# Optimization experiments

Hardware: AMD Instinct MI355X
Metric: run time of the kernel (lower is better)

The kernel has to match this reference:

```python
import jax, jax.numpy as jnp
import numpy as np

NUM_CLASSES = 50000
FEAT_DIM = 256
BATCH = 131072
LAMBDA_CENT = 0.5
EPS = 1e-12  # matches F.normalize default eps


def setup_inputs() -> dict:
    key = jax.random.key(0)
    k1, k2, k3 = jax.random.split(key, 3)
    features = jax.random.normal(k1, (BATCH, FEAT_DIM), dtype=jnp.float32)
    labels = jax.random.randint(k2, (BATCH,), 0, NUM_CLASSES)
    centers = jax.random.normal(k3, (NUM_CLASSES, FEAT_DIM), dtype=jnp.float32)
    return {"features": features, "labels": labels, "centers": centers}


def reference(features, labels, centers):
    # L2 normalize rows (F.normalize, p=2, dim=1)
    norms = jnp.linalg.norm(features, axis=1, keepdims=True)
    f = features / jnp.maximum(norms, EPS)
    # gather centers per sample: [B, D]
    cb = centers[labels]
    loss_cent = jnp.sum((f - cb) ** 2) / features.shape[0]
    # training-mode center update, vectorized:
    # torch loop: delta[labels[i]] += (cb[i] - f[i]) / (1 + count(labels == labels[i]))
    cnt = jax.ops.segment_sum(jnp.ones(labels.shape, f.dtype), labels,
                              num_segments=NUM_CLASSES)  # [C]
    w = 1.0 / (1.0 + cnt[labels])  # [B]
    delta = jax.ops.segment_sum((cb - f) * w[:, None], labels,
                                num_segments=NUM_CLASSES)  # [C, D]
    new_centers = centers - LAMBDA_CENT * delta
    return loss_cent, new_centers
```

## Files before the change

kernel.cpp:

```cpp
#include <hip/hip_runtime.h>
#include <hip/hip_bf16.h>
#include <math.h>

#define BATCH   131072
#define FEAT    256
#define NCLASS  50000
#define EPS     1e-12f
#define LAMBDA  0.5f
#define CAP     32

constexpr int WPB     = 4;
constexpr int NBLK_NS = BATCH  / WPB;
constexpr int NBLK_SS = NCLASS / WPB;
constexpr int NSCAN   = (NCLASS + 255) / 256;


__device__ __forceinline__ float wave_reduce_sum(float v) {
    #pragma unroll
    for (int m = 32; m; m >>= 1) v += __shfl_xor(v, m, 64);
    return v;
}

__device__ __forceinline__ unsigned int pack_bf16(float a, float b) {
    union { __hip_bfloat162 h; unsigned int u; } cvt;
    cvt.h = __float22bfloat162_rn(make_float2(a, b));
    return cvt.u;
}

__device__ __forceinline__ float2 unpack_bf16(unsigned int u) {
    union { unsigned int u; __hip_bfloat162 h; } cvt;
    cvt.u = u;
    return __bfloat1622float2(cvt.h);
}

__global__ __launch_bounds__(256) void histo(const int* __restrict__ labels,
                                             int* __restrict__ cnt) {
    const int i = blockIdx.x * 256 + threadIdx.x;
    atomicAdd(&cnt[labels[i]], 1);
}

__global__ __launch_bounds__(256) void scan_bsum(const int* __restrict__ cnt,
                                                 int* __restrict__ bsum) {
    __shared__ int s[256];
    const int i = blockIdx.x * 256 + threadIdx.x;
    s[threadIdx.x] = (i < NCLASS) ? cnt[i] : 0;
    __syncthreads();
    for (int off = 128; off; off >>= 1) {
        if (threadIdx.x < off) s[threadIdx.x] += s[threadIdx.x + off];
        __syncthreads();
    }
    if (threadIdx.x == 0) bsum[blockIdx.x] = s[0];
}

__global__ __launch_bounds__(256) void scan_boff(const int* __restrict__ bsum,
                                                 int* __restrict__ boff) {
    __shared__ int s[256];
    const int t = threadIdx.x;
    const int v = (t < NSCAN) ? bsum[t] : 0;
    s[t] = v;
    __syncthreads();
    for (int off = 1; off < 256; off <<= 1) {
        int u = (t >= off) ? s[t - off] : 0;
        __syncthreads();
        s[t] += u;
        __syncthreads();
    }
    if (t < NSCAN) boff[t] = s[t] - v;
}

__global__ __launch_bounds__(256) void scan_final(const int* __restrict__ cnt,
                                                  const int* __restrict__ boff,
                                                  int* __restrict__ cursor) {
    __shared__ int s[256];
    const int t = threadIdx.x;
    const int i = blockIdx.x * 256 + t;
    const int v = (i < NCLASS) ? cnt[i] : 0;
    s[t] = v;
    __syncthreads();
    for (int off = 1; off < 256; off <<= 1) {
        int u = (t >= off) ? s[t - off] : 0;
        __syncthreads();
        s[t] += u;
        __syncthreads();
    }
    if (i < NCLASS) cursor[i] = s[t] - v + boff[blockIdx.x];
}

__global__ __launch_bounds__(256) void normalize_scatter(
        const float* __restrict__ feat,
        const int*   __restrict__ labels,
        int*         __restrict__ cursor,
        uint2*       __restrict__ sortedH,
        float*       __restrict__ pA) {
    const int wave = threadIdx.x >> 6;
    const int lane = threadIdx.x & 63;
    const int row  = blockIdx.x * WPB + wave;

    const float4 v = ((const float4*)(feat + (size_t)row * FEAT))[lane];
    const float ss = wave_reduce_sum(v.x*v.x + v.y*v.y + v.z*v.z + v.w*v.w);
    const float rinv = 1.0f / fmaxf(sqrtf(ss), EPS);

    int slot = 0;
    if (lane == 0) slot = atomicAdd(&cursor[labels[row]], 1);
    slot = __shfl(slot, 0, 64);

    uint2 h;
    h.x = pack_bf16(v.x * rinv, v.y * rinv);
    h.y = pack_bf16(v.z * rinv, v.w * rinv);
    sortedH[(size_t)slot * 64 + lane] = h;

    __shared__ float red[WPB];
    if (lane == 0) red[wave] = ss * rinv * rinv;
    __syncthreads();
    if (threadIdx.x == 0)
        pA[blockIdx.x] = red[0] + red[1] + red[2] + red[3];
}

__global__ __launch_bounds__(256) void segsum_update(
        const uint2* __restrict__ sortedH,
        const float* __restrict__ centers,
        const int*   __restrict__ cnt,
        const int*   __restrict__ cursor_end,
        float*       __restrict__ outc,
        float*       __restrict__ pB) {
    const int wave = threadIdx.x >> 6;
    const int lane = threadIdx.x & 63;
    const int c    = blockIdx.x * WPB + wave;

    const int n     = cnt[c];
    const int start = cursor_end[c] - n;
    const uint2* base = sortedH + (size_t)start * 64;

    float4 acc = {0.f, 0.f, 0.f, 0.f};
    for (int s = 0; s < n; s += 4) {
        const int m = n - s;
        uint2 a0 = base[(size_t)(s + 0) * 64 + lane];
        uint2 a1 = {0u,0u}, a2 = {0u,0u}, a3 = {0u,0u};
        if (m > 1) a1 = base[(size_t)(s + 1) * 64 + lane];
        if (m > 2) a2 = base[(size_t)(s + 2) * 64 + lane];
        if (m > 3) a3 = base[(size_t)(s + 3) * 64 + lane];

        const float2 x0 = unpack_bf16(a0.x), y0 = unpack_bf16(a0.y);
        const float2 x1 = unpack_bf16(a1.x), y1 = unpack_bf16(a1.y);
        const float2 x2 = unpack_bf16(a2.x), y2 = unpack_bf16(a2.y);
        const float2 x3 = unpack_bf16(a3.x), y3 = unpack_bf16(a3.y);
        acc.x += (x0.x + x1.x) + (x2.x + x3.x);
        acc.y += (x0.y + x1.y) + (x2.y + x3.y);
        acc.z += (y0.x + y1.x) + (y2.x + y3.x);
        acc.w += (y0.y + y1.y) + (y2.y + y3.y);
    }

    const float4 cv = ((const float4*)(centers + (size_t)c * FEAT))[lane];
    const float fn = (float)n;
    const float w  = 1.0f / (1.0f + fn);

    float4 nc;
    nc.x = cv.x - LAMBDA * (fn * cv.x - acc.x) * w;
    nc.y = cv.y - LAMBDA * (fn * cv.y - acc.y) * w;
    nc.z = cv.z - LAMBDA * (fn * cv.z - acc.z) * w;
    nc.w = cv.w - LAMBDA * (fn * cv.w - acc.w) * w;
    ((float4*)(outc + (size_t)c * FEAT))[lane] = nc;

    float lp = fn * (cv.x*cv.x + cv.y*cv.y + cv.z*cv.z + cv.w*cv.w)
             - 2.0f * (acc.x*cv.x + acc.y*cv.y + acc.z*cv.z + acc.w*cv.w);
    lp = wave_reduce_sum(lp);

    __shared__ float red[WPB];
    if (lane == 0) red[wave] = lp;
    __syncthreads();
    if (threadIdx.x == 0)
        pB[blockIdx.x] = red[0] + red[1] + red[2] + red[3];
}

__global__ __launch_bounds__(1024) void finish(const float* __restrict__ pA,
                                               const float* __restrict__ pB,
                                               float* __restrict__ out0) {
    float s = 0.0f;
    for (int i = threadIdx.x; i < NBLK_NS; i += 1024) s += pA[i];
    for (int i = threadIdx.x; i < NBLK_SS; i += 1024) s += pB[i];
    s = wave_reduce_sum(s);
    __shared__ float red[16];
    const int wave = threadIdx.x >> 6;
    const int lane = threadIdx.x & 63;
    if (lane == 0) red[wave] = s;
    __syncthreads();
    if (threadIdx.x == 0) {
        float t = 0.0f;
        #pragma unroll
        for (int i = 0; i < 16; ++i) t += red[i];
        out0[0] = t * (1.0f / (float)BATCH);
    }
}


__global__ __launch_bounds__(256) void scatter_bucket(const int* __restrict__ labels,
                                                      int* __restrict__ cnt,
                                                      int* __restrict__ bucket) {
    const int i = blockIdx.x * 256 + threadIdx.x;
    const int c = labels[i];
    const int slot = atomicAdd(&cnt[c], 1);
    if (slot < CAP) bucket[c * CAP + slot] = i;
}

__global__ __launch_bounds__(256) void gather_bucket(
        const float* __restrict__ feat, const float* __restrict__ centers,
        const int* __restrict__ cnt, const int* __restrict__ bucket,
        float* __restrict__ outc, float* __restrict__ pB) {
    const int wave = threadIdx.x >> 6;
    const int lane = threadIdx.x & 63;
    const int c    = blockIdx.x * WPB + wave;
    const int n = min(cnt[c], CAP);
    const int myidx = (lane < n) ? bucket[c * CAP + lane] : 0;
    float4 acc = {0.f,0.f,0.f,0.f};
    float fsum2 = 0.f;
    for (int s = 0; s < n; ++s) {
        const int r = __shfl(myidx, s, 64);
        const float4 v = ((const float4*)(feat + (size_t)r * FEAT))[lane];
        float ss = wave_reduce_sum(v.x*v.x + v.y*v.y + v.z*v.z + v.w*v.w);
        const float rinv = 1.0f / fmaxf(sqrtf(ss), EPS);
        acc.x += v.x*rinv; acc.y += v.y*rinv; acc.z += v.z*rinv; acc.w += v.w*rinv;
        fsum2 += ss * rinv * rinv;
    }
    const float4 cv = ((const float4*)(centers + (size_t)c * FEAT))[lane];
    const float fn = (float)n;
    const float w  = 1.0f / (1.0f + fn);
    float4 nc;
    nc.x = cv.x - LAMBDA * (fn*cv.x - acc.x) * w;
    nc.y = cv.y - LAMBDA * (fn*cv.y - acc.y) * w;
    nc.z = cv.z - LAMBDA * (fn*cv.z - acc.z) * w;
    nc.w = cv.w - LAMBDA * (fn*cv.w - acc.w) * w;
    ((float4*)(outc + (size_t)c * FEAT))[lane] = nc;
    float lp = fn * (cv.x*cv.x + cv.y*cv.y + cv.z*cv.z + cv.w*cv.w)
             - 2.0f * (acc.x*cv.x + acc.y*cv.y + acc.z*cv.z + acc.w*cv.w);
    lp = wave_reduce_sum(lp);
    __shared__ float red[WPB];
    if (lane == 0) red[wave] = lp + fsum2;
    __syncthreads();
    if (threadIdx.x == 0)
        pB[blockIdx.x] = red[0] + red[1] + red[2] + red[3];
}

__global__ __launch_bounds__(1024) void finishB(const float* __restrict__ pB,
                                                float* __restrict__ out0) {
    float s = 0.0f;
    for (int i = threadIdx.x; i < NBLK_SS; i += 1024) s += pB[i];
    s = wave_reduce_sum(s);
    __shared__ float red[16];
    const int wave = threadIdx.x >> 6;
    const int lane = threadIdx.x & 63;
    if (lane == 0) red[wave] = s;
    __syncthreads();
    if (threadIdx.x == 0) {
        float t = 0.0f;
        #pragma unroll
        for (int i = 0; i < 16; ++i) t += red[i];
        out0[0] = t * (1.0f / (float)BATCH);
    }
}

extern "C" void kernel_launch(void* const* d_in, const int* in_sizes, int n_in,
                              void* d_out, int out_size, void* d_ws, size_t ws_size,
                              hipStream_t stream) {
    const float* feat    = (const float*)d_in[0];
    const int*   labels  = (const int*)  d_in[1];
    const float* centers = (const float*)d_in[2];
    float* out = (float*)d_out;

    const size_t hdr = (size_t)NCLASS * 2 + 512 + NBLK_NS + NBLK_SS;
    const size_t need_fast = hdr * 4 + (size_t)BATCH * FEAT * 2;

    if (ws_size >= need_fast) {
        int*   cnt     = (int*)d_ws;
        int*   cursor  = cnt + NCLASS;
        int*   bsum    = cursor + NCLASS;
        int*   boff    = bsum + 256;
        float* pA      = (float*)(boff + 256);
        float* pB      = pA + NBLK_NS;
        uint2* sortedH = (uint2*)(pB + NBLK_SS);

        hipMemsetAsync(cnt, 0, NCLASS * sizeof(int), stream);
        histo     <<<BATCH / 256, 256, 0, stream>>>(labels, cnt);
        scan_bsum <<<NSCAN, 256, 0, stream>>>(cnt, bsum);
        scan_boff <<<1, 256, 0, stream>>>(bsum, boff);
        scan_final<<<NSCAN, 256, 0, stream>>>(cnt, boff, cursor);
        normalize_scatter<<<NBLK_NS, 256, 0, stream>>>(feat, labels, cursor,
                                                       sortedH, pA);
        segsum_update<<<NBLK_SS, 256, 0, stream>>>(sortedH, centers, cnt, cursor,
                                                   out + 1, pB);
        finish<<<1, 1024, 0, stream>>>(pA, pB, out);
    } else {
        int*   cnt    = (int*)d_ws;
        int*   bucket = cnt + NCLASS;
        float* pB     = (float*)(bucket + (size_t)NCLASS * CAP);
        hipMemsetAsync(cnt, 0, NCLASS * sizeof(int), stream);
        scatter_bucket<<<BATCH / 256, 256, 0, stream>>>(labels, cnt, bucket);
        gather_bucket <<<NBLK_SS, 256, 0, stream>>>(feat, centers, cnt, bucket,
                                                    out + 1, pB);
        finishB<<<1, 1024, 0, stream>>>(pB, out);
    }
}
```

Baseline: 294.7 us.

## Sort row indices instead of normalized bf16 features and gather rows in segsum

Replaces the normalize-and-scatter pass, which wrote a bf16 copy of every normalized feature row into label-sorted order, with a light kernel that only scatters row indices. The per-class kernel now gathers fp32 feature rows by index, normalizes them in place with a wave reduction, and accumulates both the segment sum and the squared-norm loss term. This removes a full write and re-read of the intermediate feature buffer and the bf16 rounding, at the cost of random row gathers of fp32 data and extra shuffle reductions per row inside the segmented loop.

```diff
diff --git a/kernel.cpp b/kernel.cpp
--- a/kernel.cpp
+++ b/kernel.cpp
@@ -10,7 +10,6 @@
 #define CAP     32
 
 constexpr int WPB     = 4;
-constexpr int NBLK_NS = BATCH  / WPB;
 constexpr int NBLK_SS = NCLASS / WPB;
 constexpr int NSCAN   = (NCLASS + 255) / 256;
 
@@ -19,18 +18,6 @@
     #pragma unroll
     for (int m = 32; m; m >>= 1) v += __shfl_xor(v, m, 64);
     return v;
-}
-
-__device__ __forceinline__ unsigned int pack_bf16(float a, float b) {
-    union { __hip_bfloat162 h; unsigned int u; } cvt;
-    cvt.h = __float22bfloat162_rn(make_float2(a, b));
-    return cvt.u;
-}
-
-__device__ __forceinline__ float2 unpack_bf16(unsigned int u) {
-    union { unsigned int u; __hip_bfloat162 h; } cvt;
-    cvt.u = u;
-    return __bfloat1622float2(cvt.h);
 }
 
 __global__ __launch_bounds__(256) void histo(const int* __restrict__ labels,
@@ -86,41 +73,20 @@
     if (i < NCLASS) cursor[i] = s[t] - v + boff[blockIdx.x];
 }
 
-__global__ __launch_bounds__(256) void normalize_scatter(
+__global__ __launch_bounds__(256) void scatter_idx(const int* __restrict__ labels,
+                                                   int* __restrict__ cursor,
+                                                   int* __restrict__ sIdx) {
+    const int i = blockIdx.x * 256 + threadIdx.x;
+    const int slot = atomicAdd(&cursor[labels[i]], 1);
+    sIdx[slot] = i;
+}
+
+__global__ __launch_bounds__(256) void segsum_gather(
         const float* __restrict__ feat,
-        const int*   __restrict__ labels,
-        int*         __restrict__ cursor,
-        uint2*       __restrict__ sortedH,
-        float*       __restrict__ pA) {
-    const int wave = threadIdx.x >> 6;
-    const int lane = threadIdx.x & 63;
-    const int row  = blockIdx.x * WPB + wave;
-
-    const float4 v = ((const float4*)(feat + (size_t)row * FEAT))[lane];
-    const float ss = wave_reduce_sum(v.x*v.x + v.y*v.y + v.z*v.z + v.w*v.w);
-    const float rinv = 1.0f / fmaxf(sqrtf(ss), EPS);
-
-    int slot = 0;
-    if (lane == 0) slot = atomicAdd(&cursor[labels[row]], 1);
-    slot = __shfl(slot, 0, 64);
-
-    uint2 h;
-    h.x = pack_bf16(v.x * rinv, v.y * rinv);
-    h.y = pack_bf16(v.z * rinv, v.w * rinv);
-    sortedH[(size_t)slot * 64 + lane] = h;
-
-    __shared__ float red[WPB];
-    if (lane == 0) red[wave] = ss * rinv * rinv;
-    __syncthreads();
-    if (threadIdx.x == 0)
-        pA[blockIdx.x] = red[0] + red[1] + red[2] + red[3];
-}
-
-__global__ __launch_bounds__(256) void segsum_update(
-        const uint2* __restrict__ sortedH,
         const float* __restrict__ centers,
         const int*   __restrict__ cnt,
         const int*   __restrict__ cursor_end,
+        const int*   __restrict__ sIdx,
         float*       __restrict__ outc,
         float*       __restrict__ pB) {
     const int wave = threadIdx.x >> 6;
@@ -129,25 +95,53 @@
 
     const int n     = cnt[c];
     const int start = cursor_end[c] - n;
-    const uint2* base = sortedH + (size_t)start * 64;
-
-    float4 acc = {0.f, 0.f, 0.f, 0.f};
-    for (int s = 0; s < n; s += 4) {
-        const int m = n - s;
-        uint2 a0 = base[(size_t)(s + 0) * 64 + lane];
-        uint2 a1 = {0u,0u}, a2 = {0u,0u}, a3 = {0u,0u};
-        if (m > 1) a1 = base[(size_t)(s + 1) * 64 + lane];
-        if (m > 2) a2 = base[(size_t)(s + 2) * 64 + lane];
-        if (m > 3) a3 = base[(size_t)(s + 3) * 64 + lane];
-
-        const float2 x0 = unpack_bf16(a0.x), y0 = unpack_bf16(a0.y);
-        const float2 x1 = unpack_bf16(a1.x), y1 = unpack_bf16(a1.y);
-        const float2 x2 = unpack_bf16(a2.x), y2 = unpack_bf16(a2.y);
-        const float2 x3 = unpack_bf16(a3.x), y3 = unpack_bf16(a3.y);
-        acc.x += (x0.x + x1.x) + (x2.x + x3.x);
-        acc.y += (x0.y + x1.y) + (x2.y + x3.y);
-        acc.z += (y0.x + y1.x) + (y2.x + y3.x);
-        acc.w += (y0.y + y1.y) + (y2.y + y3.y);
+
+    float4 acc   = {0.f, 0.f, 0.f, 0.f};
+    float  fsum2 = 0.f;
+
+    for (int base = 0; base < n; base += 64) {
+        const int cn = min(64, n - base);
+        int myidx = 0;
+        if (lane < cn) myidx = sIdx[start + base + lane];
+
+        for (int s = 0; s < cn; s += 4) {
+            const int m  = cn - s;
+            const int r0 = __shfl(myidx, s + 0, 64);
+            const int r1 = __shfl(myidx, s + 1, 64);
+            const int r2 = __shfl(myidx, s + 2, 64);
+            const int r3 = __shfl(myidx, s + 3, 64);
+
+            const float4 v0 = ((const float4*)(feat + (size_t)r0 * FEAT))[lane];
+            float4 v1 = {0.f,0.f,0.f,0.f}, v2 = {0.f,0.f,0.f,0.f}, v3 = {0.f,0.f,0.f,0.f};
+            if (m > 1) v1 = ((const float4*)(feat + (size_t)r1 * FEAT))[lane];
+            if (m > 2) v2 = ((const float4*)(feat + (size_t)r2 * FEAT))[lane];
+            if (m > 3) v3 = ((const float4*)(feat + (size_t)r3 * FEAT))[lane];
+
+            float a0 = v0.x*v0.x + v0.y*v0.y + v0.z*v0.z + v0.w*v0.w;
+            float a1 = v1.x*v1.x + v1.y*v1.y + v1.z*v1.z + v1.w*v1.w;
+            float a2 = v2.x*v2.x + v2.y*v2.y + v2.z*v2.z + v2.w*v2.w;
+            float a3 = v3.x*v3.x + v3.y*v3.y + v3.z*v3.z + v3.w*v3.w;
+
+            #pragma unroll
+            for (int sh = 32; sh; sh >>= 1) {
+                a0 += __shfl_xor(a0, sh, 64);
+                a1 += __shfl_xor(a1, sh, 64);
+                a2 += __shfl_xor(a2, sh, 64);
+                a3 += __shfl_xor(a3, sh, 64);
+            }
+
+            const float i0 = 1.0f / fmaxf(sqrtf(a0), EPS);
+            const float i1 = 1.0f / fmaxf(sqrtf(a1), EPS);
+            const float i2 = 1.0f / fmaxf(sqrtf(a2), EPS);
+            const float i3 = 1.0f / fmaxf(sqrtf(a3), EPS);
+
+            acc.x += v0.x*i0 + v1.x*i1 + v2.x*i2 + v3.x*i3;
+            acc.y += v0.y*i0 + v1.y*i1 + v2.y*i2 + v3.y*i3;
+            acc.z += v0.z*i0 + v1.z*i1 + v2.z*i2 + v3.z*i3;
+            acc.w += v0.w*i0 + v1.w*i1 + v2.w*i2 + v3.w*i3;
+
+            fsum2 += (a0*i0)*i0 + (a1*i1)*i1 + (a2*i2)*i2 + (a3*i3)*i3;
+        }
     }
 
     const float4 cv = ((const float4*)(centers + (size_t)c * FEAT))[lane];
@@ -166,17 +160,15 @@
     lp = wave_reduce_sum(lp);
 
     __shared__ float red[WPB];
-    if (lane == 0) red[wave] = lp;
+    if (lane == 0) red[wave] = lp + fsum2;
     __syncthreads();
     if (threadIdx.x == 0)
         pB[blockIdx.x] = red[0] + red[1] + red[2] + red[3];
 }
 
-__global__ __launch_bounds__(1024) void finish(const float* __restrict__ pA,
-                                               const float* __restrict__ pB,
+__global__ __launch_bounds__(1024) void finish(const float* __restrict__ pB,
                                                float* __restrict__ out0) {
     float s = 0.0f;
-    for (int i = threadIdx.x; i < NBLK_NS; i += 1024) s += pA[i];
     for (int i = threadIdx.x; i < NBLK_SS; i += 1024) s += pB[i];
     s = wave_reduce_sum(s);
     __shared__ float red[16];
@@ -266,28 +258,25 @@
     const float* centers = (const float*)d_in[2];
     float* out = (float*)d_out;
 
-    const size_t hdr = (size_t)NCLASS * 2 + 512 + NBLK_NS + NBLK_SS;
-    const size_t need_fast = hdr * 4 + (size_t)BATCH * FEAT * 2;
+    const size_t need_fast = ((size_t)NCLASS * 2 + 512 + NBLK_SS + BATCH) * 4;
 
     if (ws_size >= need_fast) {
-        int*   cnt     = (int*)d_ws;
-        int*   cursor  = cnt + NCLASS;
-        int*   bsum    = cursor + NCLASS;
-        int*   boff    = bsum + 256;
-        float* pA      = (float*)(boff + 256);
-        float* pB      = pA + NBLK_NS;
-        uint2* sortedH = (uint2*)(pB + NBLK_SS);
+        int*   cnt    = (int*)d_ws;
+        int*   cursor = cnt + NCLASS;
+        int*   bsum   = cursor + NCLASS;
+        int*   boff   = bsum + 256;
+        float* pB     = (float*)(boff + 256);
+        int*   sIdx   = (int*)(pB + NBLK_SS);
 
         hipMemsetAsync(cnt, 0, NCLASS * sizeof(int), stream);
-        histo     <<<BATCH / 256, 256, 0, stream>>>(labels, cnt);
-        scan_bsum <<<NSCAN, 256, 0, stream>>>(cnt, bsum);
-        scan_boff <<<1, 256, 0, stream>>>(bsum, boff);
-        scan_final<<<NSCAN, 256, 0, stream>>>(cnt, boff, cursor);
-        normalize_scatter<<<NBLK_NS, 256, 0, stream>>>(feat, labels, cursor,
-                                                       sortedH, pA);
-        segsum_update<<<NBLK_SS, 256, 0, stream>>>(sortedH, centers, cnt, cursor,
-                                                   out + 1, pB);
-        finish<<<1, 1024, 0, stream>>>(pA, pB, out);
+        histo      <<<BATCH / 256, 256, 0, stream>>>(labels, cnt);
+        scan_bsum  <<<NSCAN, 256, 0, stream>>>(cnt, bsum);
+        scan_boff  <<<1, 256, 0, stream>>>(bsum, boff);
+        scan_final <<<NSCAN, 256, 0, stream>>>(cnt, boff, cursor);
+        scatter_idx<<<BATCH / 256, 256, 0, stream>>>(labels, cursor, sIdx);
+        segsum_gather<<<NBLK_SS, 256, 0, stream>>>(feat, centers, cnt, cursor,
+                                                   sIdx, out + 1, pB);
+        finish<<<1, 1024, 0, stream>>>(pB, out);
     } else {
         int*   cnt    = (int*)d_ws;
         int*   bucket = cnt + NCLASS;
```

Result: faster. 277.7 us (-5.8%).

## Scatter row indices and norms instead of bf16 rows; gather fp32 features in segsum

Applied to the files above, without the earlier changes.

The normalize kernel no longer writes a bf16 copy of every normalized row into a label-sorted buffer. It only records the row index and inverse norm per sorted slot. The segment-sum kernel then gathers the original fp32 feature rows by index, broadcasting indices through shuffles, and scales them by the stored inverse norm. This removes the 64MB bf16 write and re-read, but it adds a second 128MB random-gather read of the features. In exchange it improves precision by dropping the bf16 rounding.

```diff
diff --git a/kernel.cpp b/kernel.cpp
--- a/kernel.cpp
+++ b/kernel.cpp
@@ -19,18 +19,6 @@
     #pragma unroll
     for (int m = 32; m; m >>= 1) v += __shfl_xor(v, m, 64);
     return v;
-}
-
-__device__ __forceinline__ unsigned int pack_bf16(float a, float b) {
-    union { __hip_bfloat162 h; unsigned int u; } cvt;
-    cvt.h = __float22bfloat162_rn(make_float2(a, b));
-    return cvt.u;
-}
-
-__device__ __forceinline__ float2 unpack_bf16(unsigned int u) {
-    union { unsigned int u; __hip_bfloat162 h; } cvt;
-    cvt.u = u;
-    return __bfloat1622float2(cvt.h);
 }
 
 __global__ __launch_bounds__(256) void histo(const int* __restrict__ labels,
@@ -86,11 +74,12 @@
     if (i < NCLASS) cursor[i] = s[t] - v + boff[blockIdx.x];
 }
 
-__global__ __launch_bounds__(256) void normalize_scatter(
+__global__ __launch_bounds__(256) void norm_scatter(
         const float* __restrict__ feat,
         const int*   __restrict__ labels,
         int*         __restrict__ cursor,
-        uint2*       __restrict__ sortedH,
+        int*         __restrict__ sIdx,
+        float*       __restrict__ rinvS,
         float*       __restrict__ pA) {
     const int wave = threadIdx.x >> 6;
     const int lane = threadIdx.x & 63;
@@ -100,14 +89,11 @@
     const float ss = wave_reduce_sum(v.x*v.x + v.y*v.y + v.z*v.z + v.w*v.w);
     const float rinv = 1.0f / fmaxf(sqrtf(ss), EPS);
 
-    int slot = 0;
-    if (lane == 0) slot = atomicAdd(&cursor[labels[row]], 1);
-    slot = __shfl(slot, 0, 64);
-
-    uint2 h;
-    h.x = pack_bf16(v.x * rinv, v.y * rinv);
-    h.y = pack_bf16(v.z * rinv, v.w * rinv);
-    sortedH[(size_t)slot * 64 + lane] = h;
+    if (lane == 0) {
+        const int slot = atomicAdd(&cursor[labels[row]], 1);
+        sIdx[slot]  = row;
+        rinvS[slot] = rinv;
+    }
 
     __shared__ float red[WPB];
     if (lane == 0) red[wave] = ss * rinv * rinv;
@@ -116,11 +102,13 @@
         pA[blockIdx.x] = red[0] + red[1] + red[2] + red[3];
 }
 
-__global__ __launch_bounds__(256) void segsum_update(
-        const uint2* __restrict__ sortedH,
+__global__ __launch_bounds__(256) void segsum_gather2(
+        const float* __restrict__ feat,
         const float* __restrict__ centers,
         const int*   __restrict__ cnt,
         const int*   __restrict__ cursor_end,
+        const int*   __restrict__ sIdx,
+        const float* __restrict__ rinvS,
         float*       __restrict__ outc,
         float*       __restrict__ pB) {
     const int wave = threadIdx.x >> 6;
@@ -129,25 +117,30 @@
 
     const int n     = cnt[c];
     const int start = cursor_end[c] - n;
-    const uint2* base = sortedH + (size_t)start * 64;
 
     float4 acc = {0.f, 0.f, 0.f, 0.f};
-    for (int s = 0; s < n; s += 4) {
-        const int m = n - s;
-        uint2 a0 = base[(size_t)(s + 0) * 64 + lane];
-        uint2 a1 = {0u,0u}, a2 = {0u,0u}, a3 = {0u,0u};
-        if (m > 1) a1 = base[(size_t)(s + 1) * 64 + lane];
-        if (m > 2) a2 = base[(size_t)(s + 2) * 64 + lane];
-        if (m > 3) a3 = base[(size_t)(s + 3) * 64 + lane];
-
-        const float2 x0 = unpack_bf16(a0.x), y0 = unpack_bf16(a0.y);
-        const float2 x1 = unpack_bf16(a1.x), y1 = unpack_bf16(a1.y);
-        const float2 x2 = unpack_bf16(a2.x), y2 = unpack_bf16(a2.y);
-        const float2 x3 = unpack_bf16(a3.x), y3 = unpack_bf16(a3.y);
-        acc.x += (x0.x + x1.x) + (x2.x + x3.x);
-        acc.y += (x0.y + x1.y) + (x2.y + x3.y);
-        acc.z += (y0.x + y1.x) + (y2.x + y3.x);
-        acc.w += (y0.y + y1.y) + (y2.y + y3.y);
+
+    for (int base = 0; base < n; base += 64) {
+        const int cn = min(64, n - base);
+        int   myidx = 0;
+        float myrv  = 0.f;
+        if (lane < cn) {
+            myidx = sIdx [start + base + lane];
+            myrv  = rinvS[start + base + lane];
+        }
+
+        for (int s = 0; s < cn; s += 8) {
+            #pragma unroll
+            for (int k = 0; k < 8; ++k) {
+                const int   r  = __shfl(myidx, s + k, 64);
+                const float rv = __shfl(myrv,  s + k, 64);
+                const float4 v = ((const float4*)(feat + (size_t)r * FEAT))[lane];
+                acc.x += v.x * rv;
+                acc.y += v.y * rv;
+                acc.z += v.z * rv;
+                acc.w += v.w * rv;
+            }
+        }
     }
 
     const float4 cv = ((const float4*)(centers + (size_t)c * FEAT))[lane];
@@ -266,27 +259,28 @@
     const float* centers = (const float*)d_in[2];
     float* out = (float*)d_out;
 
-    const size_t hdr = (size_t)NCLASS * 2 + 512 + NBLK_NS + NBLK_SS;
-    const size_t need_fast = hdr * 4 + (size_t)BATCH * FEAT * 2;
+    const size_t need_fast =
+        ((size_t)NCLASS * 2 + 512 + NBLK_NS + NBLK_SS + (size_t)BATCH * 2) * 4;
 
     if (ws_size >= need_fast) {
-        int*   cnt     = (int*)d_ws;
-        int*   cursor  = cnt + NCLASS;
-        int*   bsum    = cursor + NCLASS;
-        int*   boff    = bsum + 256;
-        float* pA      = (float*)(boff + 256);
-        float* pB      = pA + NBLK_NS;
-        uint2* sortedH = (uint2*)(pB + NBLK_SS);
+        int*   cnt    = (int*)d_ws;
+        int*   cursor = cnt + NCLASS;
+        int*   bsum   = cursor + NCLASS;
+        int*   boff   = bsum + 256;
+        float* pA     = (float*)(boff + 256);
+        float* pB     = pA + NBLK_NS;
+        int*   sIdx   = (int*)(pB + NBLK_SS);
+        float* rinvS  = (float*)(sIdx + BATCH);
 
         hipMemsetAsync(cnt, 0, NCLASS * sizeof(int), stream);
-        histo     <<<BATCH / 256, 256, 0, stream>>>(labels, cnt);
-        scan_bsum <<<NSCAN, 256, 0, stream>>>(cnt, bsum);
-        scan_boff <<<1, 256, 0, stream>>>(bsum, boff);
-        scan_final<<<NSCAN, 256, 0, stream>>>(cnt, boff, cursor);
-        normalize_scatter<<<NBLK_NS, 256, 0, stream>>>(feat, labels, cursor,
-                                                       sortedH, pA);
-        segsum_update<<<NBLK_SS, 256, 0, stream>>>(sortedH, centers, cnt, cursor,
-                                                   out + 1, pB);
+        histo      <<<BATCH / 256, 256, 0, stream>>>(labels, cnt);
+        scan_bsum  <<<NSCAN, 256, 0, stream>>>(cnt, bsum);
+        scan_boff  <<<1, 256, 0, stream>>>(bsum, boff);
+        scan_final <<<NSCAN, 256, 0, stream>>>(cnt, boff, cursor);
+        norm_scatter<<<NBLK_NS, 256, 0, stream>>>(feat, labels, cursor,
+                                                  sIdx, rinvS, pA);
+        segsum_gather2<<<NBLK_SS, 256, 0, stream>>>(feat, centers, cnt, cursor,
+                                                    sIdx, rinvS, out + 1, pB);
         finish<<<1, 1024, 0, stream>>>(pA, pB, out);
     } else {
         int*   cnt    = (int*)d_ws;
```

Result: no change. 294.8 us (+0.0%).
